# Optimization experiments

Hardware: AMD Instinct MI355X
Metric: run time of the kernel (lower is better)

The kernel has to match this reference:

```python
import jax, jax.numpy as jnp
import numpy as np

B, T = 64, 4096
K = 67            # 25 body + 21 + 21 hand keypoints
D = 256           # first_layer_size
C = 7             # num_classes
THR = 0.1         # confidence_threshold
EPS = 1e-5        # BatchNorm eps


def setup_inputs() -> dict:
    key = jax.random.key(0)
    ks = jax.random.split(key, 8)
    body = jax.random.normal(ks[0], (B, T, 75), dtype=jnp.float32)
    hand_right = jax.random.normal(ks[1], (B, T, 63), dtype=jnp.float32)
    hand_left = jax.random.normal(ks[2], (B, T, 63), dtype=jnp.float32)
    length = jax.random.randint(ks[3], (B,), 1, T + 1, dtype=jnp.int64)
    W1 = jax.random.normal(ks[4], (2 * K, D), dtype=jnp.float32) * 0.05
    b1 = jnp.zeros((D,), dtype=jnp.float32)
    gamma = jnp.ones((D,), dtype=jnp.float32)
    beta = jnp.zeros((D,), dtype=jnp.float32)
    Wc = jax.random.normal(ks[5], (D, C), dtype=jnp.float32) * 0.05
    bc = jnp.zeros((C,), dtype=jnp.float32)
    return {"body": body, "hand_right": hand_right, "hand_left": hand_left,
            "length": length, "W1": W1, "b1": b1, "gamma": gamma,
            "beta": beta, "Wc": Wc, "bc": bc}


def reference(body, hand_right, hand_left, length, W1, b1, gamma, beta, Wc, bc):
    # concat keypoint streams -> [B, T, 3K] -> [B, T, K, 3]
    feats = jnp.concatenate([body, hand_right, hand_left], axis=2)
    feats = feats.reshape(feats.shape[0], feats.shape[1], -1, 3)
    x, y, conf = feats[..., 0], feats[..., 1], feats[..., 2]
    conf = (conf > THR).astype(feats.dtype)
    # gate coords by confidence, flatten to [B, T, 2K]
    pos = jnp.stack([x * conf, y * conf], axis=3)
    pos = pos.reshape(pos.shape[0], pos.shape[1], -1)
    # static MLP: Linear + ReLU -> [B, T, D]
    sf = jax.nn.relu(jnp.einsum("btf,fd->btd", pos, W1) + b1)
    # masked max pool over valid timesteps (vectorized segment-max)
    mask = jnp.arange(sf.shape[1])[None, :] < length[:, None]      # [B, T]
    pooled = jnp.max(jnp.where(mask[:, :, None], sf, -jnp.inf), axis=1)  # [B, D]
    # BatchNorm1d (training mode: batch statistics)
    mean = pooled.mean(axis=0)
    var = pooled.var(axis=0)
    bn = (pooled - mean) / jnp.sqrt(var + EPS) * gamma + beta
    # classifier
    return bn @ Wc + bc
```

## Files before the change

### kernel.cpp

```cpp
#include <hip/hip_runtime.h>
#include <hip/hip_bf16.h>

#define B_   64
#define T_   4096
#define K_   67
#define F_   134
#define FP_  160
#define D_   256
#define C_   7
#define THR_ 0.1f
#define EPS_ 1e-5f

typedef __bf16 bf16x8 __attribute__((ext_vector_type(8)));
typedef float  f32x4  __attribute__((ext_vector_type(4)));

typedef __attribute__((address_space(1))) const unsigned int guint;
typedef __attribute__((address_space(3))) unsigned int luint;


__device__ __forceinline__ int get_len(const int* L, int b) {
    return (L[1] == 0) ? L[2 * b] : L[b];
}

__global__ void convert_w1(const float* __restrict__ W1, __bf16* __restrict__ W1bf) {
    __shared__ float tile[32][33];
    const int d0 = blockIdx.x * 32, f0 = blockIdx.y * 32;
    const int tx = threadIdx.x & 31, ty = threadIdx.x >> 5;
#pragma unroll
    for (int r = 0; r < 32; r += 8) {
        int f = f0 + ty + r;
        tile[ty + r][tx] = (f < F_) ? W1[f * D_ + d0 + tx] : 0.f;
    }
    __syncthreads();
#pragma unroll
    for (int r = 0; r < 32; r += 8) {
        int d = d0 + ty + r;
        W1bf[d * FP_ + f0 + tx] = (__bf16)tile[tx][ty + r];
    }
}

__global__ __launch_bounds__(256, 3)
void fused_mlp_pool(const float* __restrict__ body,
                    const float* __restrict__ hr,
                    const float* __restrict__ hl,
                    const int*   __restrict__ length,
                    const float* __restrict__ b1,
                    const __bf16* __restrict__ W1bf,
                    float* __restrict__ pooled)
{
    const int b = blockIdx.y;
    const int len = get_len(length, b);
    const int t0 = blockIdx.x * 32;
    if (t0 >= len) return;

    __shared__ __align__(16) float  raw[6432];
    __shared__ __align__(16) __bf16 As[10 * 512];

    const int tid  = threadIdx.x;
    const int wave = tid >> 6;
    const int lane = tid & 63;
    const int quad = lane >> 4;
    const int l16  = lane & 15;
    const int dbase = wave * 64;

    const long rowb = (long)b * T_;
    const float* bodyt = body + (rowb + t0) * 75;
    const float* hrt   = hr   + (rowb + t0) * 63;
    const float* hlt   = hl   + (rowb + t0) * 63;

    for (int i = wave; i < 9; i += 4)
        __builtin_amdgcn_global_load_lds(
            (guint*)(bodyt + i * 256 + lane * 4),
            (luint*)((char*)raw + i * 1024 + lane * 16), 16, 0, 0);
    for (int i = wave; i < 7; i += 4)
        __builtin_amdgcn_global_load_lds(
            (guint*)(hrt + i * 256 + lane * 4),
            (luint*)((char*)raw + 9600 + i * 1024 + lane * 16), 16, 0, 0);
    for (int i = wave; i < 7; i += 4)
        __builtin_amdgcn_global_load_lds(
            (guint*)(hlt + i * 256 + lane * 4),
            (luint*)((char*)raw + 17664 + i * 1024 + lane * 16), 16, 0, 0);

    if (tid < 136) {
        const float* g; int loff;
        if (tid < 24)      { g = bodyt + 2304 + tid * 4;        loff = 2304 + tid * 4; }
        else if (tid < 80) { g = hrt + 1792 + (tid - 24) * 4;   loff = 4192 + (tid - 24) * 4; }
        else               { g = hlt + 1792 + (tid - 80) * 4;   loff = 6208 + (tid - 80) * 4; }
        *(float4*)(raw + loff) = *(const float4*)g;
    }

    bf16x8 bfrag[4][5];
    float  b1v[4];
#pragma unroll
    for (int n = 0; n < 4; n++) {
        int d = dbase + n * 16 + l16;
        const __bf16* p = W1bf + d * FP_ + quad * 8;
#pragma unroll
        for (int kt = 0; kt < 5; kt++)
            bfrag[n][kt] = *(const bf16x8*)(p + kt * 32);
        b1v[n] = b1[d];
    }

    for (int i = tid; i < 416; i += 256) {
        int t = i & 31, kp = 67 + (i >> 5);
        int w = ((t >> 4) * 5 + (kp >> 4)) * 256 + (((kp >> 2) & 3) * 16 + (t & 15)) * 4 + (kp & 3);
        ((unsigned int*)As)[w] = 0u;
    }
    __syncthreads();

#pragma unroll
    for (int it = 0; it < 8; it++) {
        int idx = it * 256 + tid;
        int t = (((idx >> 5) & 3) << 3) | ((idx >> 2) & 7);
        int k = (((idx >> 7) & 15) << 2) | (idx & 3);
        int roff;
        if (k < 25)      roff = t * 75 + 3 * k;
        else if (k < 46) roff = 2400 + t * 63 + 3 * (k - 25);
        else             roff = 4416 + t * 63 + 3 * (k - 46);
        float x = raw[roff], y = raw[roff + 1], cf = raw[roff + 2];
        if (!(cf > THR_)) { x = 0.f; y = 0.f; }
        unsigned short ux = __builtin_bit_cast(unsigned short, (__bf16)x);
        unsigned short uy = __builtin_bit_cast(unsigned short, (__bf16)y);
        int w = ((t >> 4) * 5 + (k >> 4)) * 256 + (((k >> 2) & 3) * 16 + (t & 15)) * 4 + (k & 3);
        ((unsigned int*)As)[w] = (unsigned int)ux | ((unsigned int)uy << 16);
    }
    if (tid < 96) {
        int t = tid & 31, k = 64 + (tid >> 5);
        int roff = 4416 + t * 63 + 3 * (k - 46);
        float x = raw[roff], y = raw[roff + 1], cf = raw[roff + 2];
        if (!(cf > THR_)) { x = 0.f; y = 0.f; }
        unsigned short ux = __builtin_bit_cast(unsigned short, (__bf16)x);
        unsigned short uy = __builtin_bit_cast(unsigned short, (__bf16)y);
        int w = ((t >> 4) * 5 + (k >> 4)) * 256 + (((k >> 2) & 3) * 16 + (t & 15)) * 4 + (k & 3);
        ((unsigned int*)As)[w] = (unsigned int)ux | ((unsigned int)uy << 16);
    }
    __syncthreads();

    f32x4 acc[2][4];
#pragma unroll
    for (int m = 0; m < 2; m++)
#pragma unroll
        for (int n = 0; n < 4; n++)
            acc[m][n] = (f32x4){0.f, 0.f, 0.f, 0.f};

#pragma unroll
    for (int kt = 0; kt < 5; kt++) {
#pragma unroll
        for (int m = 0; m < 2; m++) {
            bf16x8 a = *(const bf16x8*)(As + (m * 5 + kt) * 512 + lane * 8);
#pragma unroll
            for (int n = 0; n < 4; n++)
                acc[m][n] = __builtin_amdgcn_mfma_f32_16x16x32_bf16(a, bfrag[n][kt], acc[m][n], 0, 0, 0);
        }
    }

    float runmax[4] = {0.f, 0.f, 0.f, 0.f};
#pragma unroll
    for (int m = 0; m < 2; m++) {
        int trow0 = t0 + m * 16 + quad * 4;
#pragma unroll
        for (int r = 0; r < 4; r++) {
            bool valid = (trow0 + r) < len;
#pragma unroll
            for (int n = 0; n < 4; n++) {
                float v = acc[m][n][r] + b1v[n];
                v = (v > 0.f) ? v : 0.f;
                runmax[n] = (valid && v > runmax[n]) ? v : runmax[n];
            }
        }
    }
#pragma unroll
    for (int n = 0; n < 4; n++) {
        float r = runmax[n];
        r = fmaxf(r, __shfl_xor(r, 16, 64));
        r = fmaxf(r, __shfl_xor(r, 32, 64));
        if (quad == n) {
            atomicMax((unsigned int*)(pooled + b * D_ + dbase + n * 16 + l16),
                      __float_as_uint(r));
        }
    }
}

__global__ void bn_classifier(const float* __restrict__ pooled,
                              const float* __restrict__ gamma,
                              const float* __restrict__ beta,
                              const float* __restrict__ Wc,
                              const float* __restrict__ bc,
                              float* __restrict__ out)
{
    __shared__ float scale_s[D_], shift_s[D_];
    const int tid = threadIdx.x;
    float s = 0.f, ss = 0.f;
#pragma unroll 8
    for (int b = 0; b < B_; b++) {
        float v = pooled[b * D_ + tid];
        s += v; ss += v * v;
    }
    float mean = s * (1.f / B_);
    float var  = ss * (1.f / B_) - mean * mean;
    var = fmaxf(var, 0.f);
    float sc = gamma[tid] * rsqrtf(var + EPS_);
    scale_s[tid] = sc;
    shift_s[tid] = beta[tid] - mean * sc;

    const int wv = tid >> 6, ln = tid & 63;
    float wcr[4][C_];
#pragma unroll
    for (int j = 0; j < 4; j++)
#pragma unroll
        for (int c = 0; c < C_; c++)
            wcr[j][c] = Wc[(ln * 4 + j) * C_ + c];
    __syncthreads();

    for (int b = wv * 16; b < wv * 16 + 16; b++) {
        float4 v = *(const float4*)(pooled + b * D_ + ln * 4);
        float q[4];
        q[0] = v.x * scale_s[ln * 4 + 0] + shift_s[ln * 4 + 0];
        q[1] = v.y * scale_s[ln * 4 + 1] + shift_s[ln * 4 + 1];
        q[2] = v.z * scale_s[ln * 4 + 2] + shift_s[ln * 4 + 2];
        q[3] = v.w * scale_s[ln * 4 + 3] + shift_s[ln * 4 + 3];
        float p[C_];
#pragma unroll
        for (int c = 0; c < C_; c++) p[c] = 0.f;
#pragma unroll
        for (int j = 0; j < 4; j++)
#pragma unroll
            for (int c = 0; c < C_; c++)
                p[c] += q[j] * wcr[j][c];
#pragma unroll
        for (int c = 0; c < C_; c++) {
#pragma unroll
            for (int off = 1; off < 64; off <<= 1)
                p[c] += __shfl_xor(p[c], off, 64);
        }
        if (ln == 0) {
#pragma unroll
            for (int c = 0; c < C_; c++)
                out[b * C_ + c] = p[c] + bc[c];
        }
    }
}

extern "C" void kernel_launch(void* const* d_in, const int* in_sizes, int n_in,
                              void* d_out, int out_size, void* d_ws, size_t ws_size,
                              hipStream_t stream) {
    const float* body   = (const float*)d_in[0];
    const float* hr     = (const float*)d_in[1];
    const float* hl     = (const float*)d_in[2];
    const int*   length = (const int*)  d_in[3];
    const float* W1     = (const float*)d_in[4];
    const float* b1     = (const float*)d_in[5];
    const float* gamma  = (const float*)d_in[6];
    const float* beta   = (const float*)d_in[7];
    const float* Wc     = (const float*)d_in[8];
    const float* bc     = (const float*)d_in[9];
    float* out = (float*)d_out;

    float*  pooled = (float*)d_ws;
    __bf16* W1bf   = (__bf16*)((char*)d_ws + 65536);

    hipMemsetAsync(d_ws, 0, 65536, stream);
    convert_w1<<<dim3(8, 5), dim3(256), 0, stream>>>(W1, W1bf);
    fused_mlp_pool<<<dim3(128, B_), dim3(256), 0, stream>>>(body, hr, hl, length, b1, W1bf, pooled);
    bn_classifier<<<dim3(1), dim3(256), 0, stream>>>(pooled, gamma, beta, Wc, bc, out);
}
```

Measured before the change: 238.0 us.

## Make MLP-pool kernel persistent over time tiles with double-buffered async LDS loads

The grid shrinks from 128 to 16 blocks per batch row, and each block loops over time tiles with a stride of 16. The next tile's raw keypoints are prefetched into a second LDS buffer with global_load_lds, guarded by hand-written vmcnt waits, while the current tile is converted and multiplied. W1 fragments and the per-thread index math are loaded and computed once per block instead of once per tile. The aim is to hide global load latency and spread the per-block setup over more tiles. The cost is double the raw LDS footprint, a lower occupancy target, and fragile hand-counted vmcnt values; the smaller grid also risks poorer load balance across CUs.

```diff
diff --git a/kernel.cpp b/kernel.cpp
--- a/kernel.cpp
+++ b/kernel.cpp
@@ -10,6 +10,7 @@
 #define C_   7
 #define THR_ 0.1f
 #define EPS_ 1e-5f
+#define NXB_ 16
 
 typedef __bf16 bf16x8 __attribute__((ext_vector_type(8)));
 typedef float  f32x4  __attribute__((ext_vector_type(4)));
@@ -39,7 +40,7 @@
     }
 }
 
-__global__ __launch_bounds__(256, 3)
+__global__ __launch_bounds__(256, 2)
 void fused_mlp_pool(const float* __restrict__ body,
                     const float* __restrict__ hr,
                     const float* __restrict__ hl,
@@ -48,12 +49,12 @@
                     const __bf16* __restrict__ W1bf,
                     float* __restrict__ pooled)
 {
-    const int b = blockIdx.y;
+    const int b   = blockIdx.y;
     const int len = get_len(length, b);
-    const int t0 = blockIdx.x * 32;
-    if (t0 >= len) return;
-
-    __shared__ __align__(16) float  raw[6432];
+    const int nt  = (len + 31) >> 5;
+    if ((int)blockIdx.x >= nt) return;
+
+    __shared__ __align__(16) float  raw[2][6432];
     __shared__ __align__(16) __bf16 As[10 * 512];
 
     const int tid  = threadIdx.x;
@@ -64,30 +65,30 @@
     const int dbase = wave * 64;
 
     const long rowb = (long)b * T_;
-    const float* bodyt = body + (rowb + t0) * 75;
-    const float* hrt   = hr   + (rowb + t0) * 63;
-    const float* hlt   = hl   + (rowb + t0) * 63;
-
-    for (int i = wave; i < 9; i += 4)
-        __builtin_amdgcn_global_load_lds(
-            (guint*)(bodyt + i * 256 + lane * 4),
-            (luint*)((char*)raw + i * 1024 + lane * 16), 16, 0, 0);
-    for (int i = wave; i < 7; i += 4)
-        __builtin_amdgcn_global_load_lds(
-            (guint*)(hrt + i * 256 + lane * 4),
-            (luint*)((char*)raw + 9600 + i * 1024 + lane * 16), 16, 0, 0);
-    for (int i = wave; i < 7; i += 4)
-        __builtin_amdgcn_global_load_lds(
-            (guint*)(hlt + i * 256 + lane * 4),
-            (luint*)((char*)raw + 17664 + i * 1024 + lane * 16), 16, 0, 0);
-
-    if (tid < 136) {
-        const float* g; int loff;
-        if (tid < 24)      { g = bodyt + 2304 + tid * 4;        loff = 2304 + tid * 4; }
-        else if (tid < 80) { g = hrt + 1792 + (tid - 24) * 4;   loff = 4192 + (tid - 24) * 4; }
-        else               { g = hlt + 1792 + (tid - 80) * 4;   loff = 6208 + (tid - 80) * 4; }
-        *(float4*)(raw + loff) = *(const float4*)g;
-    }
+
+    auto stage = [&](int jt, int bufi) {
+        const float* bodyt = body + (rowb + (long)jt * 32) * 75;
+        const float* hrt   = hr   + (rowb + (long)jt * 32) * 63;
+        const float* hlt   = hl   + (rowb + (long)jt * 32) * 63;
+        char* rw = (char*)raw[bufi];
+        for (int i = wave; i < 10; i += 4) {
+            int off = i * 256 + lane * 4;
+            if (off < 2400)
+                __builtin_amdgcn_global_load_lds((guint*)(bodyt + off),
+                                                 (luint*)(rw + off * 4), 16, 0, 0);
+        }
+        for (int i = wave; i < 8; i += 4) {
+            int off = i * 256 + lane * 4;
+            if (off < 2016) {
+                __builtin_amdgcn_global_load_lds((guint*)(hrt + off),
+                                                 (luint*)(rw + 9600 + off * 4), 16, 0, 0);
+                __builtin_amdgcn_global_load_lds((guint*)(hlt + off),
+                                                 (luint*)(rw + 17664 + off * 4), 16, 0, 0);
+            }
+        }
+    };
+
+    stage(blockIdx.x, 0);
 
     bf16x8 bfrag[4][5];
     float  b1v[4];
@@ -101,74 +102,105 @@
         b1v[n] = b1[d];
     }
 
+    int roffv[8], wv[8];
+    {
+        const int t  = ((tid >> 5) & 3) * 8 + ((tid >> 2) & 7);
+        const int kb = ((tid >> 7) & 1) * 4 + (tid & 3);
+#pragma unroll
+        for (int it = 0; it < 8; it++) {
+            int k = it * 8 + kb;
+            roffv[it] = (k < 25) ? t * 75 + 3 * k
+                       : (k < 46) ? 2400 + t * 63 + 3 * (k - 25)
+                                  : 4416 + t * 63 + 3 * (k - 46);
+            wv[it] = ((t >> 4) * 5 + (k >> 4)) * 256
+                   + (((k >> 2) & 3) * 16 + (t & 15)) * 4 + (k & 3);
+        }
+    }
+    int roff_c = 0, w_c = 0;
+    if (tid < 96) {
+        int t = tid & 31, k = 64 + (tid >> 5);
+        roff_c = 4416 + t * 63 + 3 * (k - 46);
+        w_c = ((t >> 4) * 5 + (k >> 4)) * 256
+            + (((k >> 2) & 3) * 16 + (t & 15)) * 4 + (k & 3);
+    }
+
     for (int i = tid; i < 416; i += 256) {
         int t = i & 31, kp = 67 + (i >> 5);
-        int w = ((t >> 4) * 5 + (kp >> 4)) * 256 + (((kp >> 2) & 3) * 16 + (t & 15)) * 4 + (kp & 3);
+        int w = ((t >> 4) * 5 + (kp >> 4)) * 256
+              + (((kp >> 2) & 3) * 16 + (t & 15)) * 4 + (kp & 3);
         ((unsigned int*)As)[w] = 0u;
     }
-    __syncthreads();
-
-#pragma unroll
-    for (int it = 0; it < 8; it++) {
-        int idx = it * 256 + tid;
-        int t = (((idx >> 5) & 3) << 3) | ((idx >> 2) & 7);
-        int k = (((idx >> 7) & 15) << 2) | (idx & 3);
-        int roff;
-        if (k < 25)      roff = t * 75 + 3 * k;
-        else if (k < 46) roff = 2400 + t * 63 + 3 * (k - 25);
-        else             roff = 4416 + t * 63 + 3 * (k - 46);
-        float x = raw[roff], y = raw[roff + 1], cf = raw[roff + 2];
-        if (!(cf > THR_)) { x = 0.f; y = 0.f; }
-        unsigned short ux = __builtin_bit_cast(unsigned short, (__bf16)x);
-        unsigned short uy = __builtin_bit_cast(unsigned short, (__bf16)y);
-        int w = ((t >> 4) * 5 + (k >> 4)) * 256 + (((k >> 2) & 3) * 16 + (t & 15)) * 4 + (k & 3);
-        ((unsigned int*)As)[w] = (unsigned int)ux | ((unsigned int)uy << 16);
-    }
-    if (tid < 96) {
-        int t = tid & 31, k = 64 + (tid >> 5);
-        int roff = 4416 + t * 63 + 3 * (k - 46);
-        float x = raw[roff], y = raw[roff + 1], cf = raw[roff + 2];
-        if (!(cf > THR_)) { x = 0.f; y = 0.f; }
-        unsigned short ux = __builtin_bit_cast(unsigned short, (__bf16)x);
-        unsigned short uy = __builtin_bit_cast(unsigned short, (__bf16)y);
-        int w = ((t >> 4) * 5 + (k >> 4)) * 256 + (((k >> 2) & 3) * 16 + (t & 15)) * 4 + (k & 3);
-        ((unsigned int*)As)[w] = (unsigned int)ux | ((unsigned int)uy << 16);
-    }
-    __syncthreads();
-
-    f32x4 acc[2][4];
-#pragma unroll
-    for (int m = 0; m < 2; m++)
-#pragma unroll
-        for (int n = 0; n < 4; n++)
-            acc[m][n] = (f32x4){0.f, 0.f, 0.f, 0.f};
-
-#pragma unroll
-    for (int kt = 0; kt < 5; kt++) {
+
+    float runmax[4] = {0.f, 0.f, 0.f, 0.f};
+    int cur = 0;
+
+    for (int j = blockIdx.x; j < nt; j += NXB_) {
+        const bool hasnext = (j + NXB_ < nt);
+        if (hasnext) stage(j + NXB_, cur ^ 1);
+
+        if (hasnext) {
+            if (wave < 2) asm volatile("s_waitcnt vmcnt(7) lgkmcnt(0)\n\ts_barrier" ::: "memory");
+            else          asm volatile("s_waitcnt vmcnt(6) lgkmcnt(0)\n\ts_barrier" ::: "memory");
+        } else {
+            asm volatile("s_waitcnt vmcnt(0) lgkmcnt(0)\n\ts_barrier" ::: "memory");
+        }
+
+        const float* rw = raw[cur];
+#pragma unroll
+        for (int it = 0; it < 8; it++) {
+            float x = rw[roffv[it]], y = rw[roffv[it] + 1], cf = rw[roffv[it] + 2];
+            bool g = cf > THR_;
+            x = g ? x : 0.f;  y = g ? y : 0.f;
+            unsigned short ux = __builtin_bit_cast(unsigned short, (__bf16)x);
+            unsigned short uy = __builtin_bit_cast(unsigned short, (__bf16)y);
+            ((unsigned int*)As)[wv[it]] = (unsigned int)ux | ((unsigned int)uy << 16);
+        }
+        if (tid < 96) {
+            float x = rw[roff_c], y = rw[roff_c + 1], cf = rw[roff_c + 2];
+            bool g = cf > THR_;
+            x = g ? x : 0.f;  y = g ? y : 0.f;
+            unsigned short ux = __builtin_bit_cast(unsigned short, (__bf16)x);
+            unsigned short uy = __builtin_bit_cast(unsigned short, (__bf16)y);
+            ((unsigned int*)As)[w_c] = (unsigned int)ux | ((unsigned int)uy << 16);
+        }
+
+        asm volatile("s_waitcnt lgkmcnt(0)\n\ts_barrier" ::: "memory");
+
+        f32x4 acc[2][4];
+#pragma unroll
+        for (int m = 0; m < 2; m++)
+#pragma unroll
+            for (int n = 0; n < 4; n++)
+                acc[m][n] = (f32x4){0.f, 0.f, 0.f, 0.f};
+#pragma unroll
+        for (int kt = 0; kt < 5; kt++) {
+#pragma unroll
+            for (int m = 0; m < 2; m++) {
+                bf16x8 a = *(const bf16x8*)(As + (m * 5 + kt) * 512 + lane * 8);
+#pragma unroll
+                for (int n = 0; n < 4; n++)
+                    acc[m][n] = __builtin_amdgcn_mfma_f32_16x16x32_bf16(a, bfrag[n][kt], acc[m][n], 0, 0, 0);
+            }
+        }
+
+        const int tt0 = j * 32;
 #pragma unroll
         for (int m = 0; m < 2; m++) {
-            bf16x8 a = *(const bf16x8*)(As + (m * 5 + kt) * 512 + lane * 8);
-#pragma unroll
-            for (int n = 0; n < 4; n++)
-                acc[m][n] = __builtin_amdgcn_mfma_f32_16x16x32_bf16(a, bfrag[n][kt], acc[m][n], 0, 0, 0);
-        }
-    }
-
-    float runmax[4] = {0.f, 0.f, 0.f, 0.f};
-#pragma unroll
-    for (int m = 0; m < 2; m++) {
-        int trow0 = t0 + m * 16 + quad * 4;
-#pragma unroll
-        for (int r = 0; r < 4; r++) {
-            bool valid = (trow0 + r) < len;
-#pragma unroll
-            for (int n = 0; n < 4; n++) {
-                float v = acc[m][n][r] + b1v[n];
-                v = (v > 0.f) ? v : 0.f;
-                runmax[n] = (valid && v > runmax[n]) ? v : runmax[n];
+            int trow0 = tt0 + m * 16 + quad * 4;
+#pragma unroll
+            for (int r = 0; r < 4; r++) {
+                bool valid = (trow0 + r) < len;
+#pragma unroll
+                for (int n = 0; n < 4; n++) {
+                    float v = acc[m][n][r] + b1v[n];
+                    v = (v > 0.f) ? v : 0.f;
+                    runmax[n] = (valid && v > runmax[n]) ? v : runmax[n];
+                }
             }
         }
-    }
+        cur ^= 1;
+    }
+
 #pragma unroll
     for (int n = 0; n < 4; n++) {
         float r = runmax[n];
@@ -261,6 +293,6 @@
 
     hipMemsetAsync(d_ws, 0, 65536, stream);
     convert_w1<<<dim3(8, 5), dim3(256), 0, stream>>>(W1, W1bf);
-    fused_mlp_pool<<<dim3(128, B_), dim3(256), 0, stream>>>(body, hr, hl, length, b1, W1bf, pooled);
+    fused_mlp_pool<<<dim3(NXB_, B_), dim3(256), 0, stream>>>(body, hr, hl, length, b1, W1bf, pooled);
     bn_classifier<<<dim3(1), dim3(256), 0, stream>>>(pooled, gamma, beta, Wc, bc, out);
 }
```

Measured after the change: 229.4 us. -3.6%, faster.
